# Kernel optimization log

Measured on AMD Instinct MI355X. Metric: run time of the kernel, lower is better.

Reference implementation:

```python
import jax, jax.numpy as jnp
import numpy as np

B, N, D, C = 256, 256, 512, 1024
EPS = 1e-12  # F.normalize eps


def _l2norm(x):
    n = jnp.linalg.norm(x, axis=-1, keepdims=True)
    return x / jnp.maximum(n, EPS)


def setup_inputs() -> dict:
    key = jax.random.key(0)
    k1, k2, k3 = jax.random.split(key, 3)
    return {
        "image_tokens": jax.random.normal(k1, (B, N, D), dtype=jnp.float32),
        "text_features": jax.random.normal(k2, (C, D), dtype=jnp.float32),
        "log_tau": jnp.asarray(np.log(0.07), dtype=jnp.float32),
        "log_attn_tau": jnp.asarray(np.log(0.07), dtype=jnp.float32),
        "pid_labels": jax.random.randint(k3, (B,), 0, C),
    }


def reference(image_tokens, text_features, log_tau, log_attn_tau, pid_labels):
    toks = _l2norm(image_tokens.astype(jnp.float32))        # [B,N,D]
    txt = _l2norm(text_features.astype(jnp.float32))        # [C,D]
    sims = jnp.einsum('bnd,cd->bnc', toks, txt)             # [B,N,C]
    gt = pid_labels.astype(jnp.int32)
    # sims[arange(B), :, gt] -> [B,N]
    sims_gt = jnp.take_along_axis(sims, gt[:, None, None], axis=2)[..., 0]
    attn_tau = jnp.clip(jnp.exp(log_attn_tau), 0.01, 1.0)
    w = jax.nn.softmax(sims_gt / attn_tau, axis=1)          # [B,N]
    logits = jnp.einsum('bn,bnc->bc', w, sims)              # [B,C]
    tau = jnp.clip(jnp.exp(log_tau), 0.01, 1.0)
    logits = logits / tau
    # cross_entropy with label_smoothing=0.0, mean reduction
    logp = jax.nn.log_softmax(logits, axis=-1)
    nll = -jnp.take_along_axis(logp, gt[:, None], axis=1)[:, 0]
    return jnp.mean(nll)
```

## Files before the change

kernel.cpp:

```cpp
#include <hip/hip_runtime.h>
#include <math.h>

#define Bb 256
#define Nn 256
#define Dd 512
#define Cc 1024
#define KC 16
#define KD (Dd / KC)
#define BT 8
#define PR 16
#define PSTR 516

__device__ __forceinline__ float waveReduceSum(float v) {
    #pragma unroll
    for (int off = 32; off > 0; off >>= 1)
        v += __shfl_xor(v, off, 64);
    return v;
}
__device__ __forceinline__ float waveReduceMax(float v) {
    #pragma unroll
    for (int off = 32; off > 0; off >>= 1)
        v = fmaxf(v, __shfl_xor(v, off, 64));
    return v;
}

__global__ void k_prep(const float* __restrict__ txt, float* __restrict__ txt_t,
                       float* __restrict__ invc) {
    __shared__ float tile[PR * PSTR];
    __shared__ float invs[PR];
    const int c0 = blockIdx.x * PR;
    const int tid = threadIdx.x;
    #pragma unroll
    for (int i = tid; i < PR * 128; i += 256) {
        const int r = i >> 7, c4 = i & 127;
        const float4 v = *(const float4*)(txt + (size_t)(c0 + r) * Dd + c4 * 4);
        *(float4*)&tile[r * PSTR + c4 * 4] = v;
    }
    __syncthreads();
    {
        const int r = tid >> 4, k = tid & 15;
        float s = 0.f;
        #pragma unroll
        for (int i = 0; i < 32; ++i) {
            const float x = tile[r * PSTR + i * 16 + k];
            s = fmaf(x, x, s);
        }
        s += __shfl_xor(s, 1, 64);
        s += __shfl_xor(s, 2, 64);
        s += __shfl_xor(s, 4, 64);
        s += __shfl_xor(s, 8, 64);
        if (k == 0) {
            const float inv = 1.0f / fmaxf(sqrtf(s), 1e-12f);
            invs[r] = inv;
            invc[c0 + r] = inv;
        }
    }
    __syncthreads();
    {
        const int c = tid & 15;
        const int d0 = tid >> 4;
        const float inv = invs[c];
        #pragma unroll
        for (int d = d0; d < Dd; d += 16)
            txt_t[(size_t)d * Cc + c0 + c] = tile[c * PSTR + d] * inv;
    }
}

__global__ void __launch_bounds__(1024) k_attn_q(const float* __restrict__ toks,
                                                 const float* __restrict__ txt,
                                                 const float* __restrict__ invc,
                                                 const int* __restrict__ pid,
                                                 const float* __restrict__ log_attn_tau,
                                                 float* __restrict__ q) {
    const int b = blockIdx.x;
    const int tid = threadIdx.x;
    const int wv = tid >> 6;
    const int lane = tid & 63;
    __shared__ float xg[Dd];
    __shared__ float qpart_s[16][Dd];
    __shared__ float ms[16], Ss[16];
    const int g = pid[b];
    if (tid < Dd) xg[tid] = txt[(size_t)g * Dd + tid] * invc[g];
    __syncthreads();
    float at = expf(log_attn_tau[0]);
    at = fminf(fmaxf(at, 0.01f), 1.0f);
    const float iat = 1.0f / at;

    const float4 xg0 = *(const float4*)&xg[lane * 8];
    const float4 xg1 = *(const float4*)&xg[lane * 8 + 4];

    float m = -INFINITY, S = 0.0f;
    float qa[8] = {0.f, 0.f, 0.f, 0.f, 0.f, 0.f, 0.f, 0.f};

    const float* base = toks + ((size_t)b * Nn + wv * 16) * Dd + lane * 8;
    float4 t0 = *(const float4*)base;
    float4 t1 = *(const float4*)(base + 4);
    #pragma unroll 4
    for (int r = 0; r < 16; ++r) {
        float4 n0, n1;
        if (r < 15) {
            const float* p = base + (size_t)(r + 1) * Dd;
            n0 = *(const float4*)p;
            n1 = *(const float4*)(p + 4);
        }
        float dot = t0.x*xg0.x + t0.y*xg0.y + t0.z*xg0.z + t0.w*xg0.w
                  + t1.x*xg1.x + t1.y*xg1.y + t1.z*xg1.z + t1.w*xg1.w;
        float ss  = t0.x*t0.x + t0.y*t0.y + t0.z*t0.z + t0.w*t0.w
                  + t1.x*t1.x + t1.y*t1.y + t1.z*t1.z + t1.w*t1.w;
        dot = waveReduceSum(dot);
        ss = waveReduceSum(ss);
        const float inv = 1.0f / fmaxf(sqrtf(ss), 1e-12f);
        const float s = dot * inv;
        if (s > m) {
            const float sc = expf((m - s) * iat);
            S = S * sc + 1.0f;
            qa[0] = qa[0]*sc + inv*t0.x; qa[1] = qa[1]*sc + inv*t0.y;
            qa[2] = qa[2]*sc + inv*t0.z; qa[3] = qa[3]*sc + inv*t0.w;
            qa[4] = qa[4]*sc + inv*t1.x; qa[5] = qa[5]*sc + inv*t1.y;
            qa[6] = qa[6]*sc + inv*t1.z; qa[7] = qa[7]*sc + inv*t1.w;
            m = s;
        } else {
            const float e = expf((s - m) * iat);
            S += e;
            const float w = e * inv;
            qa[0] = fmaf(w, t0.x, qa[0]); qa[1] = fmaf(w, t0.y, qa[1]);
            qa[2] = fmaf(w, t0.z, qa[2]); qa[3] = fmaf(w, t0.w, qa[3]);
            qa[4] = fmaf(w, t1.x, qa[4]); qa[5] = fmaf(w, t1.y, qa[5]);
            qa[6] = fmaf(w, t1.z, qa[6]); qa[7] = fmaf(w, t1.w, qa[7]);
        }
        t0 = n0; t1 = n1;
    }
    #pragma unroll
    for (int j = 0; j < 8; ++j) qpart_s[wv][lane * 8 + j] = qa[j];
    if (lane == 0) { ms[wv] = m; Ss[wv] = S; }
    __syncthreads();
    if (tid < Dd) {
        float M = -INFINITY;
        #pragma unroll
        for (int w = 0; w < 16; ++w) M = fmaxf(M, ms[w]);
        float Stot = 0.f, acc = 0.f;
        #pragma unroll
        for (int w = 0; w < 16; ++w) {
            const float sc = expf((ms[w] - M) * iat);
            Stot = fmaf(Ss[w], sc, Stot);
            acc = fmaf(qpart_s[w][tid], sc, acc);
        }
        q[(size_t)b * Dd + tid] = acc / Stot;
    }
}

__global__ void k_logits(const float* __restrict__ q, const float* __restrict__ txt_t,
                         float* __restrict__ part) {
    const int b0 = blockIdx.x * BT;
    const int kc = blockIdx.y;
    const int d0 = kc * KD;
    const int t = threadIdx.x;
    __shared__ float qs[BT][KD];
    {
        const int j = t >> 5, d = t & 31;
        qs[j][d] = q[(size_t)(b0 + j) * Dd + d0 + d];
    }
    __syncthreads();
    const float4* xt = (const float4*)txt_t;
    float4 acc[BT];
    #pragma unroll
    for (int j = 0; j < BT; ++j) acc[j] = make_float4(0.f, 0.f, 0.f, 0.f);
    #pragma unroll 4
    for (int d = 0; d < KD; ++d) {
        const float4 x = xt[(size_t)(d0 + d) * (Cc / 4) + t];
        #pragma unroll
        for (int j = 0; j < BT; ++j) {
            const float qv = qs[j][d];
            acc[j].x = fmaf(qv, x.x, acc[j].x);
            acc[j].y = fmaf(qv, x.y, acc[j].y);
            acc[j].z = fmaf(qv, x.z, acc[j].z);
            acc[j].w = fmaf(qv, x.w, acc[j].w);
        }
    }
    float* pb = part + ((size_t)kc * Bb + b0) * Cc;
    #pragma unroll
    for (int j = 0; j < BT; ++j)
        ((float4*)(pb + (size_t)j * Cc))[t] = acc[j];
}

__global__ void k_lse(const float* __restrict__ part, const int* __restrict__ pid,
                      const float* __restrict__ log_tau, float* __restrict__ out) {
    const int b = blockIdx.x;
    const int t = threadIdx.x;
    float4 l = {0,0,0,0};
    #pragma unroll
    for (int kc = 0; kc < KC; ++kc) {
        const float4 p = ((const float4*)(part + ((size_t)kc * Bb + b) * Cc))[t];
        l.x += p.x; l.y += p.y; l.z += p.z; l.w += p.w;
    }
    float tau = expf(log_tau[0]);
    tau = fminf(fmaxf(tau, 0.01f), 1.0f);
    const float itau = 1.0f / tau;
    l.x *= itau; l.y *= itau; l.z *= itau; l.w *= itau;

    const int g = pid[b];
    __shared__ float redm[4], reds[4], sgt;
    if ((g >> 2) == t) {
        const float v[4] = {l.x, l.y, l.z, l.w};
        sgt = v[g & 3];
    }
    float m = fmaxf(fmaxf(l.x, l.y), fmaxf(l.z, l.w));
    m = waveReduceMax(m);
    if ((t & 63) == 0) redm[t >> 6] = m;
    __syncthreads();
    m = fmaxf(fmaxf(redm[0], redm[1]), fmaxf(redm[2], redm[3]));
    float e = expf(l.x - m) + expf(l.y - m) + expf(l.z - m) + expf(l.w - m);
    e = waveReduceSum(e);
    if ((t & 63) == 0) reds[t >> 6] = e;
    __syncthreads();
    if (t == 0) {
        const float S = reds[0] + reds[1] + reds[2] + reds[3];
        const float nll = m + logf(S) - sgt;
        atomicAdd(out, nll * (1.0f / (float)Bb));
    }
}

extern "C" void kernel_launch(void* const* d_in, const int* in_sizes, int n_in,
                              void* d_out, int out_size, void* d_ws, size_t ws_size,
                              hipStream_t stream) {
    const float* toks = (const float*)d_in[0];
    const float* txt = (const float*)d_in[1];
    const float* log_tau = (const float*)d_in[2];
    const float* log_attn_tau = (const float*)d_in[3];
    const int* pid = (const int*)d_in[4];
    float* out = (float*)d_out;

    float* ws = (float*)d_ws;
    float* txt_t = ws;
    float* invc  = txt_t + (size_t)Dd * Cc;
    float* q     = invc + Cc;
    float* part  = q + (size_t)Bb * Dd;

    hipMemsetAsync(out, 0, sizeof(float), stream);
    k_prep<<<Cc / PR, 256, 0, stream>>>(txt, txt_t, invc);
    k_attn_q<<<Bb, 1024, 0, stream>>>(toks, txt, invc, pid, log_attn_tau, q);
    k_logits<<<dim3(Bb / BT, KC), 256, 0, stream>>>(q, txt_t, part);
    k_lse<<<Bb, 256, 0, stream>>>(part, pid, log_tau, out);
}
```

Baseline: 221.9 us.

## Fuse logits GEMV and log-softmax into one kernel, drop memset launch

```diff
diff --git a/kernel.cpp b/kernel.cpp
--- a/kernel.cpp
+++ b/kernel.cpp
@@ -5,9 +5,6 @@
 #define Nn 256
 #define Dd 512
 #define Cc 1024
-#define KC 16
-#define KD (Dd / KC)
-#define BT 8
 #define PR 16
 #define PSTR 516
 
@@ -25,11 +22,12 @@
 }
 
 __global__ void k_prep(const float* __restrict__ txt, float* __restrict__ txt_t,
-                       float* __restrict__ invc) {
+                       float* __restrict__ invc, float* __restrict__ out) {
     __shared__ float tile[PR * PSTR];
     __shared__ float invs[PR];
     const int c0 = blockIdx.x * PR;
     const int tid = threadIdx.x;
+    if (blockIdx.x == 0 && tid == 0) out[0] = 0.0f;
     #pragma unroll
     for (int i = tid; i < PR * 128; i += 256) {
         const int r = i >> 7, c4 = i & 127;
@@ -149,75 +147,66 @@
     }
 }
 
-__global__ void k_logits(const float* __restrict__ q, const float* __restrict__ txt_t,
-                         float* __restrict__ part) {
-    const int b0 = blockIdx.x * BT;
-    const int kc = blockIdx.y;
-    const int d0 = kc * KD;
+__global__ void k_logits_lse(const float* __restrict__ q, const float* __restrict__ txt_t,
+                             const int* __restrict__ pid, const float* __restrict__ log_tau,
+                             float* __restrict__ out) {
+    const int b0 = blockIdx.x * 2;
     const int t = threadIdx.x;
-    __shared__ float qs[BT][KD];
-    {
-        const int j = t >> 5, d = t & 31;
-        qs[j][d] = q[(size_t)(b0 + j) * Dd + d0 + d];
+    __shared__ float qs[2][Dd];
+    #pragma unroll
+    for (int i = t; i < 2 * Dd; i += 256) {
+        const int j = i >> 9, d = i & (Dd - 1);
+        qs[j][d] = q[(size_t)(b0 + j) * Dd + d];
     }
     __syncthreads();
     const float4* xt = (const float4*)txt_t;
-    float4 acc[BT];
-    #pragma unroll
-    for (int j = 0; j < BT; ++j) acc[j] = make_float4(0.f, 0.f, 0.f, 0.f);
-    #pragma unroll 4
-    for (int d = 0; d < KD; ++d) {
-        const float4 x = xt[(size_t)(d0 + d) * (Cc / 4) + t];
-        #pragma unroll
-        for (int j = 0; j < BT; ++j) {
-            const float qv = qs[j][d];
-            acc[j].x = fmaf(qv, x.x, acc[j].x);
-            acc[j].y = fmaf(qv, x.y, acc[j].y);
-            acc[j].z = fmaf(qv, x.z, acc[j].z);
-            acc[j].w = fmaf(qv, x.w, acc[j].w);
-        }
-    }
-    float* pb = part + ((size_t)kc * Bb + b0) * Cc;
-    #pragma unroll
-    for (int j = 0; j < BT; ++j)
-        ((float4*)(pb + (size_t)j * Cc))[t] = acc[j];
-}
-
-__global__ void k_lse(const float* __restrict__ part, const int* __restrict__ pid,
-                      const float* __restrict__ log_tau, float* __restrict__ out) {
-    const int b = blockIdx.x;
-    const int t = threadIdx.x;
-    float4 l = {0,0,0,0};
-    #pragma unroll
-    for (int kc = 0; kc < KC; ++kc) {
-        const float4 p = ((const float4*)(part + ((size_t)kc * Bb + b) * Cc))[t];
-        l.x += p.x; l.y += p.y; l.z += p.z; l.w += p.w;
+    float4 a0 = {0,0,0,0}, a1 = {0,0,0,0};
+    #pragma unroll 8
+    for (int d = 0; d < Dd; ++d) {
+        const float4 x = xt[(size_t)d * (Cc / 4) + t];
+        const float q0 = qs[0][d];
+        const float q1 = qs[1][d];
+        a0.x = fmaf(q0, x.x, a0.x); a0.y = fmaf(q0, x.y, a0.y);
+        a0.z = fmaf(q0, x.z, a0.z); a0.w = fmaf(q0, x.w, a0.w);
+        a1.x = fmaf(q1, x.x, a1.x); a1.y = fmaf(q1, x.y, a1.y);
+        a1.z = fmaf(q1, x.z, a1.z); a1.w = fmaf(q1, x.w, a1.w);
     }
     float tau = expf(log_tau[0]);
     tau = fminf(fmaxf(tau, 0.01f), 1.0f);
     const float itau = 1.0f / tau;
-    l.x *= itau; l.y *= itau; l.z *= itau; l.w *= itau;
-
-    const int g = pid[b];
-    __shared__ float redm[4], reds[4], sgt;
-    if ((g >> 2) == t) {
-        const float v[4] = {l.x, l.y, l.z, l.w};
-        sgt = v[g & 3];
-    }
-    float m = fmaxf(fmaxf(l.x, l.y), fmaxf(l.z, l.w));
-    m = waveReduceMax(m);
-    if ((t & 63) == 0) redm[t >> 6] = m;
-    __syncthreads();
-    m = fmaxf(fmaxf(redm[0], redm[1]), fmaxf(redm[2], redm[3]));
-    float e = expf(l.x - m) + expf(l.y - m) + expf(l.z - m) + expf(l.w - m);
-    e = waveReduceSum(e);
-    if ((t & 63) == 0) reds[t >> 6] = e;
-    __syncthreads();
-    if (t == 0) {
-        const float S = reds[0] + reds[1] + reds[2] + reds[3];
-        const float nll = m + logf(S) - sgt;
-        atomicAdd(out, nll * (1.0f / (float)Bb));
-    }
+    a0.x *= itau; a0.y *= itau; a0.z *= itau; a0.w *= itau;
+    a1.x *= itau; a1.y *= itau; a1.z *= itau; a1.w *= itau;
+
+    __shared__ float redm[4], reds[4], sgt0, sgt1;
+    const int g0 = pid[b0], g1 = pid[b0 + 1];
+    if ((g0 >> 2) == t) {
+        const float v[4] = {a0.x, a0.y, a0.z, a0.w};
+        sgt0 = v[g0 & 3];
+    }
+    if ((g1 >> 2) == t) {
+        const float v[4] = {a1.x, a1.y, a1.z, a1.w};
+        sgt1 = v[g1 & 3];
+    }
+    float nll_sum = 0.f;
+    #pragma unroll
+    for (int j = 0; j < 2; ++j) {
+        const float4 l = j == 0 ? a0 : a1;
+        float m = fmaxf(fmaxf(l.x, l.y), fmaxf(l.z, l.w));
+        m = waveReduceMax(m);
+        if ((t & 63) == 0) redm[t >> 6] = m;
+        __syncthreads();
+        m = fmaxf(fmaxf(redm[0], redm[1]), fmaxf(redm[2], redm[3]));
+        float e = expf(l.x - m) + expf(l.y - m) + expf(l.z - m) + expf(l.w - m);
+        e = waveReduceSum(e);
+        if ((t & 63) == 0) reds[t >> 6] = e;
+        __syncthreads();
+        if (t == 0) {
+            const float S = reds[0] + reds[1] + reds[2] + reds[3];
+            nll_sum += m + logf(S) - (j == 0 ? sgt0 : sgt1);
+        }
+        __syncthreads();
+    }
+    if (t == 0) atomicAdd(out, nll_sum * (1.0f / (float)Bb));
 }
 
 extern "C" void kernel_launch(void* const* d_in, const int* in_sizes, int n_in,
@@ -234,11 +223,8 @@
     float* txt_t = ws;
     float* invc  = txt_t + (size_t)Dd * Cc;
     float* q     = invc + Cc;
-    float* part  = q + (size_t)Bb * Dd;
-
-    hipMemsetAsync(out, 0, sizeof(float), stream);
-    k_prep<<<Cc / PR, 256, 0, stream>>>(txt, txt_t, invc);
+
+    k_prep<<<Cc / PR, 256, 0, stream>>>(txt, txt_t, invc, out);
     k_attn_q<<<Bb, 1024, 0, stream>>>(toks, txt, invc, pid, log_attn_tau, q);
-    k_logits<<<dim3(Bb / BT, KC), 256, 0, stream>>>(q, txt_t, part);
-    k_lse<<<Bb, 256, 0, stream>>>(part, pid, log_tau, out);
-}
+    k_logits_lse<<<Bb / 2, 256, 0, stream>>>(q, txt_t, pid, log_tau, out);
+}
```

Result: slower. 233.6 us (+5.3%).
